# Kernel optimization log

Measured on AMD Instinct MI355X. Metric: run time of the kernel, lower is better.

The kernel has to match this reference:

```python
import jax, jax.numpy as jnp
import numpy as np
from jax import lax

H = 64      # hidden_size
VOC = 512   # num_embedding
L = 2       # num_layers


def layernorm(x, g, b, eps=1e-5):
    mu = jnp.mean(x, axis=-1, keepdims=True)
    var = jnp.mean((x - mu) ** 2, axis=-1, keepdims=True)
    return (x - mu) * lax.rsqrt(var + eps) * g + b


def conv3d(x, w, b):
    # x: [B, U, V, W, Cin] (channels-last), w: [3,3,3,Cin,Cout]
    return lax.conv_general_dilated(
        x, w, (1, 1, 1), 'SAME',
        dimension_numbers=('NDHWC', 'DHWIO', 'NDHWC')) + b


def setup_inputs() -> dict:
    key = jax.random.key(0)
    ks = jax.random.split(key, 8)
    f = lambda k, s, sc: jax.random.normal(k, s, jnp.float32) * sc
    return {
        'code': jax.random.randint(ks[0], (2, 5, 1, 8, 8, 8), 0, VOC),
        'ncode': jax.random.randint(ks[1], (2, 3, 1, 8, 8, 8), 0, VOC),
        'emb': f(ks[2], (VOC, H), 0.02),
        'win': f(ks[3], (L, 3, 3, 3, H, 4 * H), 0.05),
        'bin_': jnp.zeros((L, 4 * H), jnp.float32),
        'gin_w': jnp.ones((L, 4 * H), jnp.float32),
        'gin_b': jnp.zeros((L, 4 * H), jnp.float32),
        'wh': f(ks[4], (L, 3, 3, 3, H, 4 * H), 0.05),
        'bh': jnp.zeros((L, 4 * H), jnp.float32),
        'gh_w': jnp.ones((L, 4 * H), jnp.float32),
        'gh_b': jnp.zeros((L, 4 * H), jnp.float32),
        'w1': f(ks[5], (H, H), 0.05),
        'b1': jnp.zeros((H,), jnp.float32),
        'ln_g': jnp.ones((H,), jnp.float32),
        'ln_b': jnp.zeros((H,), jnp.float32),
        'w2': f(ks[6], (H, VOC), 0.05),
        'b2': jnp.zeros((VOC,), jnp.float32),
    }


def _forward(code, ncode, emb, win, bin_, gin_w, gin_b, wh, bh, gh_w, gh_b,
             w1, b1, ln_g, ln_b, w2, b2):
    N, Sn, C, U, V, W = ncode.shape
    x = jnp.concatenate([code, ncode[:, :-1]], axis=1)  # [N,S,C,U,V,W]
    S = x.shape[1]
    x = jnp.transpose(x, (0, 2, 1, 3, 4, 5)).reshape(N * C, S, U, V, W)
    h = emb[x]  # [NC, S, U, V, W, H]
    Hd = h.shape[-1]
    for i in range(L):
        # input-path conv is recurrence-free: batch it over all timesteps
        gi = layernorm(conv3d(h.reshape(N * C * S, U, V, W, Hd), win[i], bin_[i]),
                       gin_w[i], gin_b[i])
        gi = jnp.moveaxis(gi.reshape(N * C, S, U, V, W, 4 * Hd), 1, 0)  # [S,NC,U,V,W,4H]

        def step(carry, g, i=i):
            hx, cx = carry
            gates = g + layernorm(conv3d(hx, wh[i], bh[i]), gh_w[i], gh_b[i])
            ig, fg, cg, og = jnp.split(gates, 4, axis=-1)
            cx = jax.nn.sigmoid(fg) * cx + jax.nn.sigmoid(ig) * jnp.tanh(cg)
            hx = jax.nn.sigmoid(og) * jnp.tanh(cx)
            return (hx, cx), hx

        z = jnp.zeros((N * C, U, V, W, Hd), h.dtype)
        _, ys = lax.scan(step, (z, z), gi)
        h = jnp.moveaxis(ys, 0, 1)  # [NC,S,U,V,W,H]
    h = h[:, -Sn:].reshape(N, C, Sn, U, V, W, Hd)
    h = jnp.transpose(h, (0, 2, 1, 3, 4, 5, 6))  # [N,Sn,C,U,V,W,H]
    z = jax.nn.gelu(layernorm(h @ w1 + b1, ln_g, ln_b), approximate=False)
    logits = z @ w2 + b2  # [N,Sn,C,U,V,W,VOC]
    score = jnp.transpose(logits, (0, 6, 1, 2, 3, 4, 5))  # [N,VOC,Sn,C,U,V,W]
    logp = jax.nn.log_softmax(logits, axis=-1)
    loss = -jnp.mean(jnp.take_along_axis(logp, ncode[..., None], axis=-1))
    pred = jnp.argmax(score, axis=1)
    return score, loss, pred


def reference(code, ncode, emb, win, bin_, gin_w, gin_b, wh, bh, gh_w, gh_b,
              w1, b1, ln_g, ln_b, w2, b2):
    return _forward(code, ncode, emb, win, bin_, gin_w, gin_b, wh, bh,
                    gh_w, gh_b, w1, b1, ln_g, ln_b, w2, b2)
```

## Files before the change

kernel.cpp:

```cpp
#include <hip/hip_runtime.h>


typedef _Float16 f16;
typedef _Float16 f16x8 __attribute__((ext_vector_type(8)));
typedef float    f32x4 __attribute__((ext_vector_type(4)));

#define WSTRIDE 442368
#define WPT     884736
#define XSP     65536
#define HSP     458752
#define GPART   262144

__device__ __forceinline__ float wred_sum(float v) {
    #pragma unroll
    for (int o = 32; o > 0; o >>= 1) v += __shfl_down(v, o, 64);
    return __shfl(v, 0, 64);
}
__device__ __forceinline__ float fsig(float x)  { return 1.f / (1.f + __expf(-x)); }
__device__ __forceinline__ float ftanh(float x) { return 1.f - 2.f / (__expf(2.f*x) + 1.f); }

__global__ __launch_bounds__(256) void prep_kernel(
    const int* __restrict__ code, const int* __restrict__ ncode,
    const float* __restrict__ emb, f16* __restrict__ h,
    const float* __restrict__ win, const float* __restrict__ wh,
    f16* __restrict__ wp)
{
    if (blockIdx.x < 1792) {
        int e = blockIdx.x * 256 + threadIdx.x;
        int ch = e & 63;
        int pos = e >> 6;
        int vox = pos & 511;
        int t = pos >> 9;
        int s = t % 7, nc = t / 7;
        int tok = (s < 5) ? code[(nc*5 + s)*512 + vox]
                          : ncode[(nc*3 + (s-5))*512 + vox];
        float x = emb[tok*64 + ch];
        f16 hi = (f16)x;
        h[(size_t)pos*128 + ch]      = hi;
        h[(size_t)pos*128 + 64 + ch] = (f16)(x - (float)hi);
    } else {
        int b = blockIdx.x - 1792;
        int tensor = b / 27, tap = b % 27;
        const float* src = ((tensor & 1) ? wh : win) + (tensor >> 1) * WSTRIDE
                         + tap * 16384;
        int co = threadIdx.x;
        int sw = co & 7;
        #pragma unroll
        for (int hs = 0; hs < 2; ++hs) {
            f16* dst = wp + (((size_t)tensor*27 + tap)*2 + hs)*16384 + co*64;
            #pragma unroll
            for (int j = 0; j < 4; ++j) {
                f16x8 hi8, lo8;
                #pragma unroll
                for (int m = 0; m < 8; ++m) {
                    float w = src[(hs*32 + j*8 + m)*256 + co] * 64.f;
                    f16 hv = (f16)w;
                    hi8[m] = hv;
                    lo8[m] = (f16)(w - (float)hv);
                }
                *(f16x8*)(dst + ((j     ^ sw))*8) = hi8;
                *(f16x8*)(dst + (((4+j) ^ sw))*8) = lo8;
            }
        }
    }
}

struct MJob { const f16* x; const f16* w; float* y; };
struct MJobs { MJob j[8]; };

__global__ __launch_bounds__(256, 4) void conv_mfma_kernel(MJobs js)
{
    const MJob J = js.j[blockIdx.y];
    __shared__ float4 smem[2048];
    f16* wbuf = (f16*)smem;

    const int bx = blockIdx.x;
    const int cog = bx & 3, u = (bx >> 2) & 7, slab = (bx >> 5) & 1;
    const int ah = (bx >> 6) & 1, kb = bx >> 7;
    const int t = threadIdx.x, wid = t >> 6, l = t & 63;
    const int lv = (l >> 3) & 1, lw = l & 7, khi = l >> 4;

    const int gid = kb*4 + wid;
    const int g0  = (gid < 6) ? gid*4 : 24 + (gid - 6)*3;
    const int cnt = (gid < 6) ? 4 : 3;

    const f16* xbase = J.x + (size_t)slab * HSP;
    const f16* wjob  = J.w + (size_t)cog * 4096;
    f16* wmine = wbuf + wid * 4096;

    f16x8 wreg[8];
    auto wload = [&](int k) {
        const f16* src = wjob + (size_t)k * 16384 + l * 8;
        #pragma unroll
        for (int i = 0; i < 8; ++i) wreg[i] = *(const f16x8*)(src + i * 512);
    };
    auto wstore = [&]() {
        f16* dst = wmine + l * 8;
        #pragma unroll
        for (int i = 0; i < 8; ++i) *(f16x8*)(dst + i * 512) = wreg[i];
    };

    wload(g0); wstore();

    f32x4 acc[2][4] = {};
    for (int q = 0; q < cnt; ++q) {
        const int k = g0 + q;
        if (q + 1 < cnt) wload(k + 1);
        const int tap = k >> 1, hs = k & 1;
        const int du = tap / 9, rr = tap % 9, dv = rr / 3, dw = rr % 3;
        const int uu = u + du - 1;
        const bool uok = (unsigned)uu < 8u;
        const f16* xrow[2]; bool ok[2];
        #pragma unroll
        for (int aa = 0; aa < 2; ++aa) {
            int vs = (ah*2 + aa)*2 + lv + dv - 1, ws = lw + dw - 1;
            ok[aa] = uok && (unsigned)vs < 8u && (unsigned)ws < 8u;
            xrow[aa] = xbase + ((size_t)(uu*64 + vs*8 + ws) << 7) + khi*8;
        }
        const f16* wrow = wmine + (l & 15)*64;
        const int schi = ((khi    ) ^ lw) * 8;
        const int sclo = ((4 + khi) ^ lw) * 8;
        f16x8 ahi[2], alo[2], bhi[4], blo[4];
        #pragma unroll
        for (int aa = 0; aa < 2; ++aa) {
            f16x8 v = {0,0,0,0,0,0,0,0}, v2 = v;
            if (ok[aa]) {
                v  = *(const f16x8*)(xrow[aa] + hs*32);
                v2 = *(const f16x8*)(xrow[aa] + 64 + hs*32);
            }
            ahi[aa] = v; alo[aa] = v2;
        }
        #pragma unroll
        for (int n = 0; n < 4; ++n) {
            bhi[n] = *(const f16x8*)(wrow + n*1024 + schi);
            blo[n] = *(const f16x8*)(wrow + n*1024 + sclo);
        }
        #pragma unroll
        for (int aa = 0; aa < 2; ++aa)
            #pragma unroll
            for (int n = 0; n < 4; ++n)
                acc[aa][n] = __builtin_amdgcn_mfma_f32_16x16x32_f16(
                    ahi[aa], bhi[n], acc[aa][n], 0, 0, 0);
        #pragma unroll
        for (int aa = 0; aa < 2; ++aa)
            #pragma unroll
            for (int n = 0; n < 4; ++n)
                acc[aa][n] = __builtin_amdgcn_mfma_f32_16x16x32_f16(
                    alo[aa], bhi[n], acc[aa][n], 0, 0, 0);
        #pragma unroll
        for (int aa = 0; aa < 2; ++aa)
            #pragma unroll
            for (int n = 0; n < 4; ++n)
                acc[aa][n] = __builtin_amdgcn_mfma_f32_16x16x32_f16(
                    ahi[aa], blo[n], acc[aa][n], 0, 0, 0);
        if (q + 1 < cnt) wstore();
    }

    f32x4* red = (f32x4*)smem;
    {
        f32x4* mine = red + (size_t)(wid * 64 + l) * 8;
        #pragma unroll
        for (int aa = 0; aa < 2; ++aa)
            #pragma unroll
            for (int n = 0; n < 4; ++n)
                mine[(aa * 4 + n) ^ lw] = acc[aa][n];
    }
    __syncthreads();
    {
        float* yp = J.y + (size_t)kb * GPART;
        const int aa = (t >> 7) & 1, nsel = (t >> 6) & 1, ll = t & 63;
        #pragma unroll
        for (int ni = 0; ni < 2; ++ni) {
            const int n = nsel*2 + ni;
            const int ch = (aa * 4 + n) ^ (ll & 7);
            f32x4 sv = red[(0 * 64 + ll) * 8 + ch]
                     + red[(1 * 64 + ll) * 8 + ch]
                     + red[(2 * 64 + ll) * 8 + ch]
                     + red[(3 * 64 + ll) * 8 + ch];
            const int co = cog * 64 + n * 16 + (ll & 15);
            #pragma unroll
            for (int r = 0; r < 4; ++r) {
                int vox = (ah*2 + aa) * 16 + (ll >> 4) * 4 + r;
                yp[(size_t)(slab * 512 + u * 64 + vox) * 256 + co]
                    = sv[r] * 0.015625f;
            }
        }
    }
}

struct GJob {
    const float* gi;
    const float* gh;
    const float* bin; const float* bhb;
    const float* ginw; const float* ginb;
    const float* ghw;  const float* ghb;
    float* cx; f16* h16; int k; int k0;
};
__global__ __launch_bounds__(256) void gates_step_kernel(GJob ja, GJob jb)
{
    const GJob J = (blockIdx.y == 0) ? ja : jb;
    const int wid = threadIdx.x >> 6, lane = threadIdx.x & 63;
    const int row = blockIdx.x * 4 + wid;
    const int nc = row >> 9, vox = row & 511;

    const float* g = J.gi + (size_t)row*256;
    float a0 = g[lane]             + g[GPART+lane]
             + g[2*GPART+lane]     + g[3*GPART+lane]     + J.bin[lane];
    float a1 = g[64+lane]          + g[GPART+64+lane]
             + g[2*GPART+64+lane]  + g[3*GPART+64+lane]  + J.bin[64+lane];
    float a2 = g[128+lane]         + g[GPART+128+lane]
             + g[2*GPART+128+lane] + g[3*GPART+128+lane] + J.bin[128+lane];
    float a3 = g[192+lane]         + g[GPART+192+lane]
             + g[2*GPART+192+lane] + g[3*GPART+192+lane] + J.bin[192+lane];
    float mu1 = wred_sum(a0+a1+a2+a3) * (1.f/256.f);
    float d0=a0-mu1, d1=a1-mu1, d2=a2-mu1, d3=a3-mu1;
    float v1 = wred_sum(d0*d0+d1*d1+d2*d2+d3*d3) * (1.f/256.f);
    float rs1 = rsqrtf(v1 + 1e-5f);

    float b0, b1, b2, b3;
    if (J.k0) {
        b0 = J.bhb[lane]; b1 = J.bhb[64+lane];
        b2 = J.bhb[128+lane]; b3 = J.bhb[192+lane];
    } else {
        const float* hh = J.gh + (size_t)row*256;
        b0 = hh[lane]             + hh[GPART+lane]
           + hh[2*GPART+lane]     + hh[3*GPART+lane]     + J.bhb[lane];
        b1 = hh[64+lane]          + hh[GPART+64+lane]
           + hh[2*GPART+64+lane]  + hh[3*GPART+64+lane]  + J.bhb[64+lane];
        b2 = hh[128+lane]         + hh[GPART+128+lane]
           + hh[2*GPART+128+lane] + hh[3*GPART+128+lane] + J.bhb[128+lane];
        b3 = hh[192+lane]         + hh[GPART+192+lane]
           + hh[2*GPART+192+lane] + hh[3*GPART+192+lane] + J.bhb[192+lane];
    }
    float mu2 = wred_sum(b0+b1+b2+b3) * (1.f/256.f);
    float e0=b0-mu2, e1=b1-mu2, e2=b2-mu2, e3=b3-mu2;
    float v2 = wred_sum(e0*e0+e1*e1+e2*e2+e3*e3) * (1.f/256.f);
    float rs2 = rsqrtf(v2 + 1e-5f);

    float Ig = d0*rs1*J.ginw[lane]     + J.ginb[lane]     + e0*rs2*J.ghw[lane]     + J.ghb[lane];
    float Fg = d1*rs1*J.ginw[64+lane]  + J.ginb[64+lane]  + e1*rs2*J.ghw[64+lane]  + J.ghb[64+lane];
    float Cg = d2*rs1*J.ginw[128+lane] + J.ginb[128+lane] + e2*rs2*J.ghw[128+lane] + J.ghb[128+lane];
    float Og = d3*rs1*J.ginw[192+lane] + J.ginb[192+lane] + e3*rs2*J.ghw[192+lane] + J.ghb[192+lane];

    float c_old = J.k0 ? 0.f : J.cx[(size_t)row*64 + lane];
    float c_new = fsig(Fg)*c_old + fsig(Ig)*ftanh(Cg);
    float h_new = fsig(Og)*ftanh(c_new);
    J.cx[(size_t)row*64 + lane] = c_new;
    size_t hb = ((size_t)(nc*7 + J.k)*512 + vox)*128 + lane;
    f16 hi = (f16)h_new;
    J.h16[hb]      = hi;
    J.h16[hb + 64] = (f16)(h_new - (float)hi);
}

__global__ __launch_bounds__(256) void head_kernel(
    const f16* __restrict__ h,
    const float* __restrict__ w1, const float* __restrict__ b1,
    const float* __restrict__ lng, const float* __restrict__ lnb,
    const float* __restrict__ w2, const float* __restrict__ b2,
    const int* __restrict__ ncode,
    float* __restrict__ out, float* __restrict__ lossb, GJob g2)
{
    __shared__ float hsm[4][64];
    __shared__ float zv[4][64];
    __shared__ float lg[4][512];
    __shared__ float lsum[4];
    const int blk = blockIdx.x;
    const int n = blk / 384;
    const int sn = (blk / 128) % 3;
    const int vox0 = (blk & 127) * 4;
    const int t = threadIdx.x, wid = t >> 6, lane = t & 63;
    const int vox = vox0 + wid;

    if (sn == 2) {
        const int row = n*512 + vox;
        const float* g = g2.gi + (size_t)row*256;
        float a0 = g[lane]             + g[GPART+lane]
                 + g[2*GPART+lane]     + g[3*GPART+lane]     + g2.bin[lane];
        float a1 = g[64+lane]          + g[GPART+64+lane]
                 + g[2*GPART+64+lane]  + g[3*GPART+64+lane]  + g2.bin[64+lane];
        float a2 = g[128+lane]         + g[GPART+128+lane]
                 + g[2*GPART+128+lane] + g[3*GPART+128+lane] + g2.bin[128+lane];
        float a3 = g[192+lane]         + g[GPART+192+lane]
                 + g[2*GPART+192+lane] + g[3*GPART+192+lane] + g2.bin[192+lane];
        float mu1 = wred_sum(a0+a1+a2+a3) * (1.f/256.f);
        float d0=a0-mu1, d1=a1-mu1, d2=a2-mu1, d3=a3-mu1;
        float v1 = wred_sum(d0*d0+d1*d1+d2*d2+d3*d3) * (1.f/256.f);
        float rs1 = rsqrtf(v1 + 1e-5f);

        const float* hh = g2.gh + (size_t)row*256;
        float b0v = hh[lane]             + hh[GPART+lane]
                  + hh[2*GPART+lane]     + hh[3*GPART+lane]     + g2.bhb[lane];
        float b1v = hh[64+lane]          + hh[GPART+64+lane]
                  + hh[2*GPART+64+lane]  + hh[3*GPART+64+lane]  + g2.bhb[64+lane];
        float b2v = hh[128+lane]         + hh[GPART+128+lane]
                  + hh[2*GPART+128+lane] + hh[3*GPART+128+lane] + g2.bhb[128+lane];
        float b3v = hh[192+lane]         + hh[GPART+192+lane]
                  + hh[2*GPART+192+lane] + hh[3*GPART+192+lane] + g2.bhb[192+lane];
        float mu2 = wred_sum(b0v+b1v+b2v+b3v) * (1.f/256.f);
        float e0=b0v-mu2, e1=b1v-mu2, e2=b2v-mu2, e3=b3v-mu2;
        float v2 = wred_sum(e0*e0+e1*e1+e2*e2+e3*e3) * (1.f/256.f);
        float rs2 = rsqrtf(v2 + 1e-5f);

        float Ig = d0*rs1*g2.ginw[lane]     + g2.ginb[lane]     + e0*rs2*g2.ghw[lane]     + g2.ghb[lane];
        float Fg = d1*rs1*g2.ginw[64+lane]  + g2.ginb[64+lane]  + e1*rs2*g2.ghw[64+lane]  + g2.ghb[64+lane];
        float Cg = d2*rs1*g2.ginw[128+lane] + g2.ginb[128+lane] + e2*rs2*g2.ghw[128+lane] + g2.ghb[128+lane];
        float Og = d3*rs1*g2.ginw[192+lane] + g2.ginb[192+lane] + e3*rs2*g2.ghw[192+lane] + g2.ghb[192+lane];

        float c_old = g2.cx[(size_t)row*64 + lane];
        float c_new = fsig(Fg)*c_old + fsig(Ig)*ftanh(Cg);
        hsm[wid][lane] = fsig(Og)*ftanh(c_new);
    } else {
        const f16* hv = h + (size_t)((n*7 + sn + 4)*512 + vox)*128;
        hsm[wid][lane] = (float)hv[lane] + (float)hv[64 + lane];
    }

    float yva = b1[lane], yvb = 0.f;
    for (int kk = 0; kk < 64; kk += 2) {
        yva = fmaf(hsm[wid][kk],     w1[kk*64 + lane],     yva);
        yvb = fmaf(hsm[wid][kk + 1], w1[(kk+1)*64 + lane], yvb);
    }
    float yv = yva + yvb;
    float mu = wred_sum(yv) * (1.f/64.f);
    float d = yv - mu;
    float var = wred_sum(d*d) * (1.f/64.f);
    float ln = d * rsqrtf(var + 1e-5f) * lng[lane] + lnb[lane];
    zv[wid][lane] = 0.5f * ln * (1.f + erff(ln * 0.70710678118654752f));

    float l[8];
    #pragma unroll
    for (int j = 0; j < 8; ++j) l[j] = b2[j*64 + lane];
    for (int kk = 0; kk < 64; ++kk) {
        float zz = zv[wid][kk];
        #pragma unroll
        for (int j = 0; j < 8; ++j)
            l[j] = fmaf(zz, w2[kk*512 + j*64 + lane], l[j]);
    }
    #pragma unroll
    for (int j = 0; j < 8; ++j) lg[wid][j*64 + lane] = l[j];

    float m = l[0]; int mi = lane;
    #pragma unroll
    for (int j = 1; j < 8; ++j)
        if (l[j] > m) { m = l[j]; mi = j*64 + lane; }
    #pragma unroll
    for (int o = 32; o > 0; o >>= 1) {
        float om = __shfl_down(m, o, 64);
        int   oi = __shfl_down(mi, o, 64);
        if (om > m || (om == m && oi < mi)) { m = om; mi = oi; }
    }
    float maxv = __shfl(m, 0, 64);
    int   maxi = __shfl(mi, 0, 64);
    float es = 0.f;
    #pragma unroll
    for (int j = 0; j < 8; ++j) es += __expf(l[j] - maxv);
    float sum = wred_sum(es);
    if (lane == 0) {
        int target = ncode[(n*3 + sn)*512 + vox];
        float logp = lg[wid][target] - maxv - __logf(sum);
        lsum[wid] = -logp * (1.f/3072.f);
        out[1572865 + (n*3 + sn)*512 + vox] = (float)maxi;
    }

    __syncthreads();
    if (t == 0) lossb[blk] = lsum[0] + lsum[1] + lsum[2] + lsum[3];
    for (int co = t; co < 512; co += 256) {
        float4 o4 = { lg[0][co], lg[1][co], lg[2][co], lg[3][co] };
        *(float4*)(out + (size_t)((n*512 + co)*3 + sn)*512 + vox0) = o4;
    }
}

__global__ void loss_fin_kernel(const float* __restrict__ lossb,
                                float* __restrict__ out)
{
    float s = 0.f;
    for (int i = threadIdx.x; i < 768; i += 64) s += lossb[i];
    s = wred_sum(s);
    if (threadIdx.x == 0) out[1572864] = s;
}

extern "C" void kernel_launch(void* const* d_in, const int* in_sizes, int n_in,
                              void* d_out, int out_size, void* d_ws, size_t ws_size,
                              hipStream_t stream) {
    (void)in_sizes; (void)n_in; (void)out_size; (void)ws_size;
    const int*   code  = (const int*)d_in[0];
    const int*   ncode = (const int*)d_in[1];
    const float* emb   = (const float*)d_in[2];
    const float* win   = (const float*)d_in[3];
    const float* bin_  = (const float*)d_in[4];
    const float* gin_w = (const float*)d_in[5];
    const float* gin_b = (const float*)d_in[6];
    const float* wh    = (const float*)d_in[7];
    const float* bh    = (const float*)d_in[8];
    const float* gh_w  = (const float*)d_in[9];
    const float* gh_b  = (const float*)d_in[10];
    const float* w1    = (const float*)d_in[11];
    const float* b1    = (const float*)d_in[12];
    const float* ln_g  = (const float*)d_in[13];
    const float* ln_b  = (const float*)d_in[14];
    const float* w2    = (const float*)d_in[15];
    const float* b2    = (const float*)d_in[16];
    float* out = (float*)d_out;

    float* base  = (float*)d_ws;
    f16*   wp    = (f16*)base;
    f16*   h1    = (f16*)(base + 1769472);
    f16*   h2    = (f16*)(base + 2228224);
    float* gi1   = base + 2686976;
    float* gi2   = gi1 + 7*4*(size_t)GPART;
    float* ghat1 = gi2 + 4*(size_t)GPART;
    float* ghat2 = ghat1 + 4*(size_t)GPART;
    float* cx1   = ghat2 + 4*(size_t)GPART;
    float* cx2   = cx1 + 65536;
    float* lossb = base + 13303808;

    const f16* win0 = wp;
    const f16* wh0  = wp + WPT;
    const f16* win1 = wp + 2*WPT;
    const f16* wh1  = wp + 3*WPT;

    prep_kernel<<<1900, 256, 0, stream>>>(code, ncode, emb, h1, win, wh, wp);

    {
        MJobs js{};
        for (int s = 0; s < 7; ++s)
            js.j[s] = { h1 + (size_t)s*XSP, win0, gi1 + (size_t)s*4*GPART };
        conv_mfma_kernel<<<dim3(512, 7), 256, 0, stream>>>(js);
    }

    for (int s = 0; s <= 6; ++s) {
        GJob g1 = { gi1 + (size_t)s*4*GPART, ghat1, bin_, bh,
                    gin_w, gin_b, gh_w, gh_b, cx1, h1, s, s == 0 };
        GJob g2 = { gi2, ghat2, bin_ + 256, bh + 256,
                    gin_w + 256, gin_b + 256, gh_w + 256, gh_b + 256,
                    cx2, h2, s - 1, s == 1 };
        if (s == 0)
            gates_step_kernel<<<dim3(256, 1), 256, 0, stream>>>(g1, g1);
        else
            gates_step_kernel<<<dim3(256, 2), 256, 0, stream>>>(g1, g2);

        MJobs js{}; int nj = 0;
        if (s <= 5) js.j[nj++] = { h1 + (size_t)s*XSP,     wh0,  ghat1 };
        js.j[nj++]             = { h1 + (size_t)s*XSP,     win1, gi2 };
        if (s >= 1) js.j[nj++] = { h2 + (size_t)(s-1)*XSP, wh1,  ghat2 };
        conv_mfma_kernel<<<dim3(512, nj), 256, 0, stream>>>(js);
    }

    GJob g2h = { gi2, ghat2, bin_ + 256, bh + 256,
                 gin_w + 256, gin_b + 256, gh_w + 256, gh_b + 256,
                 cx2, h2, 6, 0 };
    head_kernel<<<768, 256, 0, stream>>>(h2, w1, b1, ln_g, ln_b, w2, b2,
                                         ncode, out, lossb, g2h);
    loss_fin_kernel<<<1, 64, 0, stream>>>(lossb, out);
}
```

Before: 311.1 us.

## Widen conv block tile to four row groups and use channel-planar activation layout

Each conv block now covers all four voxel row-pairs (acc[4][4]) instead of two. Every weight fragment loaded from shared memory therefore feeds twice as many MFMAs, and the grid shrinks to half the blocks. Activations move from an interleaved [vox][128] layout to a channel-group-planar layout ([16][512][8] per slab), so lanes read contiguous 8-voxel runs. The writers in prep, gates and head are updated to match. In exchange, register and shared-memory use roughly double, occupancy is capped at 2 blocks, and an extra barrier is added before the reduction.

```diff
diff --git a/kernel.cpp b/kernel.cpp
--- a/kernel.cpp
+++ b/kernel.cpp
@@ -30,14 +30,15 @@
         int ch = e & 63;
         int pos = e >> 6;
         int vox = pos & 511;
-        int t = pos >> 9;
-        int s = t % 7, nc = t / 7;
+        int slab = pos >> 9;
+        int s = slab % 7, nc = slab / 7;
         int tok = (s < 5) ? code[(nc*5 + s)*512 + vox]
                           : ncode[(nc*3 + (s-5))*512 + vox];
         float x = emb[tok*64 + ch];
         f16 hi = (f16)x;
-        h[(size_t)pos*128 + ch]      = hi;
-        h[(size_t)pos*128 + 64 + ch] = (f16)(x - (float)hi);
+        size_t sb = (size_t)slab * XSP;
+        h[sb + (ch>>3)*4096       + vox*8 + (ch&7)] = hi;
+        h[sb + ((ch>>3)+8)*4096   + vox*8 + (ch&7)] = (f16)(x - (float)hi);
     } else {
         int b = blockIdx.x - 1792;
         int tensor = b / 27, tap = b % 27;
@@ -68,15 +69,14 @@
 struct MJob { const f16* x; const f16* w; float* y; };
 struct MJobs { MJob j[8]; };
 
-__global__ __launch_bounds__(256, 4) void conv_mfma_kernel(MJobs js)
+__global__ __launch_bounds__(256, 2) void conv_mfma_kernel(MJobs js)
 {
     const MJob J = js.j[blockIdx.y];
-    __shared__ float4 smem[2048];
+    __shared__ float4 smem[4096];
     f16* wbuf = (f16*)smem;
 
     const int bx = blockIdx.x;
-    const int cog = bx & 3, u = (bx >> 2) & 7, slab = (bx >> 5) & 1;
-    const int ah = (bx >> 6) & 1, kb = bx >> 7;
+    const int cog = bx & 3, u = (bx >> 2) & 7, slab = (bx >> 5) & 1, kb = bx >> 6;
     const int t = threadIdx.x, wid = t >> 6, l = t & 63;
     const int lv = (l >> 3) & 1, lw = l & 7, khi = l >> 4;
 
@@ -102,7 +102,7 @@
 
     wload(g0); wstore();
 
-    f32x4 acc[2][4] = {};
+    f32x4 acc[4][4] = {};
     for (int q = 0; q < cnt; ++q) {
         const int k = g0 + q;
         if (q + 1 < cnt) wload(k + 1);
@@ -110,77 +110,88 @@
         const int du = tap / 9, rr = tap % 9, dv = rr / 3, dw = rr % 3;
         const int uu = u + du - 1;
         const bool uok = (unsigned)uu < 8u;
-        const f16* xrow[2]; bool ok[2];
-        #pragma unroll
-        for (int aa = 0; aa < 2; ++aa) {
-            int vs = (ah*2 + aa)*2 + lv + dv - 1, ws = lw + dw - 1;
-            ok[aa] = uok && (unsigned)vs < 8u && (unsigned)ws < 8u;
-            xrow[aa] = xbase + ((size_t)(uu*64 + vs*8 + ws) << 7) + khi*8;
+        const int choff = (khi + hs*4) * 4096;
+        const f16* xrow[4]; bool ok[4];
+        #pragma unroll
+        for (int a = 0; a < 4; ++a) {
+            int vs = a*2 + lv + dv - 1, ws = lw + dw - 1;
+            ok[a] = uok && (unsigned)vs < 8u && (unsigned)ws < 8u;
+            xrow[a] = xbase + choff + (uu*64 + vs*8 + ws)*8;
         }
         const f16* wrow = wmine + (l & 15)*64;
         const int schi = ((khi    ) ^ lw) * 8;
         const int sclo = ((4 + khi) ^ lw) * 8;
-        f16x8 ahi[2], alo[2], bhi[4], blo[4];
-        #pragma unroll
-        for (int aa = 0; aa < 2; ++aa) {
-            f16x8 v = {0,0,0,0,0,0,0,0}, v2 = v;
-            if (ok[aa]) {
-                v  = *(const f16x8*)(xrow[aa] + hs*32);
-                v2 = *(const f16x8*)(xrow[aa] + 64 + hs*32);
-            }
-            ahi[aa] = v; alo[aa] = v2;
-        }
+        f16x8 bhi[4], blo[4];
         #pragma unroll
         for (int n = 0; n < 4; ++n) {
             bhi[n] = *(const f16x8*)(wrow + n*1024 + schi);
             blo[n] = *(const f16x8*)(wrow + n*1024 + sclo);
         }
-        #pragma unroll
-        for (int aa = 0; aa < 2; ++aa)
-            #pragma unroll
-            for (int n = 0; n < 4; ++n)
-                acc[aa][n] = __builtin_amdgcn_mfma_f32_16x16x32_f16(
-                    ahi[aa], bhi[n], acc[aa][n], 0, 0, 0);
-        #pragma unroll
-        for (int aa = 0; aa < 2; ++aa)
-            #pragma unroll
-            for (int n = 0; n < 4; ++n)
-                acc[aa][n] = __builtin_amdgcn_mfma_f32_16x16x32_f16(
-                    alo[aa], bhi[n], acc[aa][n], 0, 0, 0);
-        #pragma unroll
-        for (int aa = 0; aa < 2; ++aa)
-            #pragma unroll
-            for (int n = 0; n < 4; ++n)
-                acc[aa][n] = __builtin_amdgcn_mfma_f32_16x16x32_f16(
-                    ahi[aa], blo[n], acc[aa][n], 0, 0, 0);
+        {
+            f16x8 ahi[4];
+            #pragma unroll
+            for (int a = 0; a < 4; ++a) {
+                f16x8 v = {0,0,0,0,0,0,0,0};
+                if (ok[a]) v = *(const f16x8*)(xrow[a]);
+                ahi[a] = v;
+            }
+            #pragma unroll
+            for (int a = 0; a < 4; ++a)
+                #pragma unroll
+                for (int n = 0; n < 4; ++n)
+                    acc[a][n] = __builtin_amdgcn_mfma_f32_16x16x32_f16(
+                        ahi[a], bhi[n], acc[a][n], 0, 0, 0);
+            #pragma unroll
+            for (int a = 0; a < 4; ++a)
+                #pragma unroll
+                for (int n = 0; n < 4; ++n)
+                    acc[a][n] = __builtin_amdgcn_mfma_f32_16x16x32_f16(
+                        ahi[a], blo[n], acc[a][n], 0, 0, 0);
+        }
+        {
+            f16x8 alo[4];
+            #pragma unroll
+            for (int a = 0; a < 4; ++a) {
+                f16x8 v = {0,0,0,0,0,0,0,0};
+                if (ok[a]) v = *(const f16x8*)(xrow[a] + 32768);
+                alo[a] = v;
+            }
+            #pragma unroll
+            for (int a = 0; a < 4; ++a)
+                #pragma unroll
+                for (int n = 0; n < 4; ++n)
+                    acc[a][n] = __builtin_amdgcn_mfma_f32_16x16x32_f16(
+                        alo[a], bhi[n], acc[a][n], 0, 0, 0);
+        }
         if (q + 1 < cnt) wstore();
     }
+
+    __syncthreads();
 
     f32x4* red = (f32x4*)smem;
     {
-        f32x4* mine = red + (size_t)(wid * 64 + l) * 8;
-        #pragma unroll
-        for (int aa = 0; aa < 2; ++aa)
+        f32x4* mine = red + (size_t)(wid * 64 + l) * 16;
+        #pragma unroll
+        for (int a = 0; a < 4; ++a)
             #pragma unroll
             for (int n = 0; n < 4; ++n)
-                mine[(aa * 4 + n) ^ lw] = acc[aa][n];
+                mine[(a * 4 + n) ^ (l & 15)] = acc[a][n];
     }
     __syncthreads();
     {
         float* yp = J.y + (size_t)kb * GPART;
-        const int aa = (t >> 7) & 1, nsel = (t >> 6) & 1, ll = t & 63;
-        #pragma unroll
-        for (int ni = 0; ni < 2; ++ni) {
-            const int n = nsel*2 + ni;
-            const int ch = (aa * 4 + n) ^ (ll & 7);
-            f32x4 sv = red[(0 * 64 + ll) * 8 + ch]
-                     + red[(1 * 64 + ll) * 8 + ch]
-                     + red[(2 * 64 + ll) * 8 + ch]
-                     + red[(3 * 64 + ll) * 8 + ch];
+        const int a = t >> 6, ll = t & 63;
+        #pragma unroll
+        for (int n = 0; n < 4; ++n) {
+            const int ch = (a * 4 + n) ^ (ll & 15);
+            f32x4 sv = red[(0 * 64 + ll) * 16 + ch]
+                     + red[(1 * 64 + ll) * 16 + ch]
+                     + red[(2 * 64 + ll) * 16 + ch]
+                     + red[(3 * 64 + ll) * 16 + ch];
             const int co = cog * 64 + n * 16 + (ll & 15);
             #pragma unroll
             for (int r = 0; r < 4; ++r) {
-                int vox = (ah*2 + aa) * 16 + (ll >> 4) * 4 + r;
+                int vox = a * 16 + (ll >> 4) * 4 + r;
                 yp[(size_t)(slab * 512 + u * 64 + vox) * 256 + co]
                     = sv[r] * 0.015625f;
             }
@@ -246,10 +257,10 @@
     float c_new = fsig(Fg)*c_old + fsig(Ig)*ftanh(Cg);
     float h_new = fsig(Og)*ftanh(c_new);
     J.cx[(size_t)row*64 + lane] = c_new;
-    size_t hb = ((size_t)(nc*7 + J.k)*512 + vox)*128 + lane;
+    size_t sb = (size_t)(nc*7 + J.k) * XSP;
     f16 hi = (f16)h_new;
-    J.h16[hb]      = hi;
-    J.h16[hb + 64] = (f16)(h_new - (float)hi);
+    J.h16[sb + (lane>>3)*4096     + vox*8 + (lane&7)] = hi;
+    J.h16[sb + ((lane>>3)+8)*4096 + vox*8 + (lane&7)] = (f16)(h_new - (float)hi);
 }
 
 __global__ __launch_bounds__(256) void head_kernel(
@@ -310,8 +321,9 @@
         float c_new = fsig(Fg)*c_old + fsig(Ig)*ftanh(Cg);
         hsm[wid][lane] = fsig(Og)*ftanh(c_new);
     } else {
-        const f16* hv = h + (size_t)((n*7 + sn + 4)*512 + vox)*128;
-        hsm[wid][lane] = (float)hv[lane] + (float)hv[64 + lane];
+        const f16* hv = h + (size_t)(n*7 + sn + 4) * XSP;
+        hsm[wid][lane] = (float)hv[(lane>>3)*4096     + vox*8 + (lane&7)]
+                       + (float)hv[((lane>>3)+8)*4096 + vox*8 + (lane&7)];
     }
 
     float yva = b1[lane], yvb = 0.f;
@@ -424,7 +436,7 @@
         MJobs js{};
         for (int s = 0; s < 7; ++s)
             js.j[s] = { h1 + (size_t)s*XSP, win0, gi1 + (size_t)s*4*GPART };
-        conv_mfma_kernel<<<dim3(512, 7), 256, 0, stream>>>(js);
+        conv_mfma_kernel<<<dim3(256, 7), 256, 0, stream>>>(js);
     }
 
     for (int s = 0; s <= 6; ++s) {
@@ -442,7 +454,7 @@
         if (s <= 5) js.j[nj++] = { h1 + (size_t)s*XSP,     wh0,  ghat1 };
         js.j[nj++]             = { h1 + (size_t)s*XSP,     win1, gi2 };
         if (s >= 1) js.j[nj++] = { h2 + (size_t)(s-1)*XSP, wh1,  ghat2 };
-        conv_mfma_kernel<<<dim3(512, nj), 256, 0, stream>>>(js);
+        conv_mfma_kernel<<<dim3(256, nj), 256, 0, stream>>>(js);
     }
 
     GJob g2h = { gi2, ghat2, bin_ + 256, bh + 256,
```

Result: faster. 293.0 us (-5.8%).
